# Kernel optimization log

Measured on AMD Instinct MI355X. Metric: run time of the kernel, lower is better.

Reference implementation:

```python
import jax, jax.numpy as jnp
import numpy as np

N_NODES = 100000
N_EDGES = 1000000
D_FEAT = 64


def setup_inputs() -> dict:
    key = jax.random.key(0)
    k1, k2 = jax.random.split(key)
    x = jax.random.normal(k1, (N_NODES, D_FEAT), dtype=jnp.float32)
    es = jax.random.randint(k2, (2, N_EDGES), 0, N_NODES, dtype=jnp.int32)
    return {"x": x, "es": es}


def reference(x, es):
    # message (option='o2i'): col, row = es ; x_i = x[row], x_o = x[col]
    col, row = es[0], es[1]
    x_i = x[row]                              # [E, D]
    x_o = x[col]                              # [E, D]
    msg = jnp.concatenate([x_i, x_o], axis=-1)  # [E, 2D]
    n = x.shape[0]
    # aggregate: scatter-mean over idx=col
    summed = jax.ops.segment_sum(msg, col, num_segments=n)          # [N, 2D]
    ones = jnp.ones((es.shape[1],), dtype=x.dtype)
    count = jax.ops.segment_sum(ones, col, num_segments=n)          # [N]
    count = jnp.maximum(count, 1.0)[:, None]  # clamp(min=1), broadcast
    return summed / count
```

## Files before the change

### kernel.cpp

```cpp
#include <hip/hip_runtime.h>

#define D 64
#define SH 8
#define CPB 256
#define CH 4096
#define MAXNB 512

__global__ __launch_bounds__(256) void count_scan(
    const int* __restrict__ es, int* __restrict__ btot,
    int* __restrict__ done, int* __restrict__ bbase,
    int* __restrict__ cursor, int* __restrict__ offsets,
    int NB, int E, int N) {
  __shared__ int hist[MAXNB];
  __shared__ int sctmp[256];
  __shared__ int lastflag;
  int t = threadIdx.x;
  hist[t] = 0;
  hist[t + 256] = 0;
  __syncthreads();
  int base_e = blockIdx.x * CH;
#pragma unroll
  for (int j = 0; j < 16; j++) {
    int e = base_e + t + j * 256;
    if (e < E) atomicAdd(&hist[es[e] >> SH], 1);
  }
  __syncthreads();
  for (int b = t; b < NB; b += 256) {
    int h = hist[b];
    if (h) atomicAdd(&btot[b], h);
  }
  __syncthreads();
  if (t == 0) {
    __threadfence();
    int d = atomicAdd(done, 1);
    lastflag = (d == (int)gridDim.x - 1);
  }
  __syncthreads();
  if (!lastflag) return;
  __threadfence();
  int i0 = 2 * t, i1 = 2 * t + 1;
  int h0 = (i0 < NB) ? __hip_atomic_load(&btot[i0], __ATOMIC_RELAXED,
                                         __HIP_MEMORY_SCOPE_AGENT) : 0;
  int h1 = (i1 < NB) ? __hip_atomic_load(&btot[i1], __ATOMIC_RELAXED,
                                         __HIP_MEMORY_SCOPE_AGENT) : 0;
  int pair = h0 + h1;
  sctmp[t] = pair;
  __syncthreads();
  for (int off = 1; off < 256; off <<= 1) {
    int v = (t >= off) ? sctmp[t - off] : 0;
    __syncthreads();
    sctmp[t] += v;
    __syncthreads();
  }
  int excl = sctmp[t] - pair;
  if (i0 < NB) { bbase[i0] = excl; cursor[i0] = excl; }
  if (i1 < NB) { bbase[i1] = excl + h0; cursor[i1] = excl + h0; }
  if (t == 0) { bbase[NB] = E; offsets[N] = E; }
}

__global__ __launch_bounds__(256) void scatter_res(
    const int* __restrict__ es, int* __restrict__ cursor,
    int* __restrict__ packed, int NB, int E) {
  __shared__ int hist[MAXNB];
  __shared__ int lstart[MAXNB];
  __shared__ int gbase[MAXNB];
  __shared__ int lcur[MAXNB];
  __shared__ int sctmp[256];
  __shared__ int staged[CH];
  __shared__ unsigned short bidl[CH];
  int t = threadIdx.x;
  hist[t] = 0;
  hist[t + 256] = 0;
  __syncthreads();
  int base_e = blockIdx.x * CH;
  int c[16], r[16];
#pragma unroll
  for (int j = 0; j < 16; j++) {
    int e = base_e + t + j * 256;
    if (e < E) {
      c[j] = es[e];
      r[j] = es[E + e];
      atomicAdd(&hist[c[j] >> SH], 1);
    } else {
      c[j] = -1;
    }
  }
  __syncthreads();
  int h0 = hist[2 * t], h1 = hist[2 * t + 1];
  int pair = h0 + h1;
  sctmp[t] = pair;
  __syncthreads();
  for (int off = 1; off < 256; off <<= 1) {
    int v = (t >= off) ? sctmp[t - off] : 0;
    __syncthreads();
    sctmp[t] += v;
    __syncthreads();
  }
  int excl = sctmp[t] - pair;
  lstart[2 * t] = excl;
  lstart[2 * t + 1] = excl + h0;
  lcur[2 * t] = excl;
  lcur[2 * t + 1] = excl + h0;
  for (int b = t; b < NB; b += 256) {
    int h = hist[b];
    gbase[b] = h ? atomicAdd(&cursor[b], h) : 0;
  }
  __syncthreads();
#pragma unroll
  for (int j = 0; j < 16; j++) {
    if (c[j] >= 0) {
      int b = c[j] >> SH;
      int rank = atomicAdd(&lcur[b], 1);
      staged[rank] = (r[j] << SH) | (c[j] & (CPB - 1));
      bidl[rank] = (unsigned short)b;
    }
  }
  __syncthreads();
  int nloc = min(CH, E - base_e);
  for (int i = t; i < nloc; i += 256) {
    int b = bidl[i];
    packed[gbase[b] + (i - lstart[b])] = staged[i];
  }
}

__global__ __launch_bounds__(256) void sort_cols(
    const int* __restrict__ packed, const int* __restrict__ bbase,
    int* __restrict__ offsets, int* __restrict__ sorted_rows, int N) {
  __shared__ int cnt[CPB];
  __shared__ int sctmp[256];
  __shared__ int cur[CPB];
  int b = blockIdx.x;
  int t = threadIdx.x;
  int s = bbase[b], e = bbase[b + 1];
  cnt[t] = 0;
  __syncthreads();
  for (int i = s + t; i < e; i += 256) atomicAdd(&cnt[packed[i] & (CPB - 1)], 1);
  __syncthreads();
  int v = cnt[t];
  sctmp[t] = v;
  __syncthreads();
  for (int off = 1; off < 256; off <<= 1) {
    int u = (t >= off) ? sctmp[t - off] : 0;
    __syncthreads();
    sctmp[t] += u;
    __syncthreads();
  }
  int excl = sctmp[t] - v;
  cur[t] = excl;
  int gc = (b << SH) + t;
  if (gc < N) offsets[gc] = s + excl;
  __syncthreads();
  for (int i = s + t; i < e; i += 256) {
    int p = packed[i];
    int rank = atomicAdd(&cur[p & (CPB - 1)], 1);
    sorted_rows[s + rank] = p >> SH;
  }
}

__global__ __launch_bounds__(256) void node_reduce(
    const float4* __restrict__ x4, const int* __restrict__ sorted_rows,
    const int* __restrict__ offsets, float* __restrict__ out, int N) {
  int gid = blockIdx.x * 256 + threadIdx.x;
  int node = gid >> 6;
  if (node >= N) return;
  int lane = threadIdx.x & 63;
  int eg = lane >> 4;
  int d16 = lane & 15;
  int start = offsets[node];
  int cnt = offsets[node + 1] - start;
  float4 a0 = make_float4(0.f, 0.f, 0.f, 0.f);
  float4 a1 = make_float4(0.f, 0.f, 0.f, 0.f);
  float4 a2 = make_float4(0.f, 0.f, 0.f, 0.f);
  float4 a3 = make_float4(0.f, 0.f, 0.f, 0.f);
  for (int base = 0; base < cnt; base += 16) {
    int k0 = base + eg;
    int k1 = base + 4 + eg;
    int k2 = base + 8 + eg;
    int k3 = base + 12 + eg;
    int r0 = (k0 < cnt) ? sorted_rows[start + k0] : -1;
    int r1 = (k1 < cnt) ? sorted_rows[start + k1] : -1;
    int r2 = (k2 < cnt) ? sorted_rows[start + k2] : -1;
    int r3 = (k3 < cnt) ? sorted_rows[start + k3] : -1;
    if (r0 >= 0) { float4 v = x4[(size_t)r0 * 16 + d16];
      a0.x += v.x; a0.y += v.y; a0.z += v.z; a0.w += v.w; }
    if (r1 >= 0) { float4 v = x4[(size_t)r1 * 16 + d16];
      a1.x += v.x; a1.y += v.y; a1.z += v.z; a1.w += v.w; }
    if (r2 >= 0) { float4 v = x4[(size_t)r2 * 16 + d16];
      a2.x += v.x; a2.y += v.y; a2.z += v.z; a2.w += v.w; }
    if (r3 >= 0) { float4 v = x4[(size_t)r3 * 16 + d16];
      a3.x += v.x; a3.y += v.y; a3.z += v.z; a3.w += v.w; }
  }
  a0.x += a1.x + a2.x + a3.x;
  a0.y += a1.y + a2.y + a3.y;
  a0.z += a1.z + a2.z + a3.z;
  a0.w += a1.w + a2.w + a3.w;
  a0.x += __shfl_xor(a0.x, 16); a0.y += __shfl_xor(a0.y, 16);
  a0.z += __shfl_xor(a0.z, 16); a0.w += __shfl_xor(a0.w, 16);
  a0.x += __shfl_xor(a0.x, 32); a0.y += __shfl_xor(a0.y, 32);
  a0.z += __shfl_xor(a0.z, 32); a0.w += __shfl_xor(a0.w, 32);
  float4* o4 = (float4*)(out + (size_t)node * 2 * D);
  if (eg == 0) {
    float inv = 1.0f / (float)(cnt > 0 ? cnt : 1);
    a0.x *= inv; a0.y *= inv; a0.z *= inv; a0.w *= inv;
    o4[d16] = a0;
  } else if (eg == 1) {
    float4 v = (cnt > 0) ? x4[(size_t)node * 16 + d16]
                         : make_float4(0.f, 0.f, 0.f, 0.f);
    o4[16 + d16] = v;
  }
}


__global__ __launch_bounds__(256) void edge_scatter_atomic(
    const int* __restrict__ es, const float* __restrict__ x,
    float* __restrict__ out, int* __restrict__ count, int E) {
  int gid = blockIdx.x * blockDim.x + threadIdx.x;
  int e = gid >> 6;
  int lane = gid & 63;
  if (e >= E) return;
  int c = es[e];
  int r = es[E + e];
  if (lane == 0) atomicAdd(&count[c], 1);
  float v = x[(size_t)r * D + lane];
  unsafeAtomicAdd(&out[(size_t)c * 2 * D + lane], v);
}

__global__ __launch_bounds__(256) void finalize_atomic(
    const float* __restrict__ x, float* __restrict__ out,
    const int* __restrict__ count, int N) {
  int gid = blockIdx.x * blockDim.x + threadIdx.x;
  int node = gid >> 5;
  int j4 = gid & 31;
  if (node >= N) return;
  int cnt = count[node];
  float4* out4 = (float4*)(out + (size_t)node * 2 * D);
  if (j4 < 16) {
    float4 s = out4[j4];
    float inv = 1.0f / (float)(cnt > 0 ? cnt : 1);
    s.x *= inv; s.y *= inv; s.z *= inv; s.w *= inv;
    out4[j4] = s;
  } else {
    float4 v;
    if (cnt > 0) {
      const float4* x4 = (const float4*)(x + (size_t)node * D);
      v = x4[j4 - 16];
    } else {
      v = make_float4(0.f, 0.f, 0.f, 0.f);
    }
    out4[j4] = v;
  }
}

extern "C" void kernel_launch(void* const* d_in, const int* in_sizes, int n_in,
                              void* d_out, int out_size, void* d_ws, size_t ws_size,
                              hipStream_t stream) {
  const float* x = (const float*)d_in[0];
  const int* es = (const int*)d_in[1];
  int N = in_sizes[0] / D;
  int E = in_sizes[1] / 2;
  float* out = (float*)d_out;

  int NB = (N + CPB - 1) >> SH;
  int NBLK = (E + CH - 1) / CH;
  size_t need = ((size_t)NB + 1 + (NB + 1) + NB + ((size_t)N + 1) +
                 2 * (size_t)E) * sizeof(int);
  if (NB > MAXNB || ws_size < need) {
    int* count = (int*)d_ws;
    hipMemsetAsync(count, 0, (size_t)N * sizeof(int), stream);
    hipMemsetAsync(out, 0, (size_t)N * 2 * D * sizeof(float), stream);
    long long t1 = (long long)E * 64;
    edge_scatter_atomic<<<(int)((t1 + 255) / 256), 256, 0, stream>>>(es, x, out, count, E);
    long long t2 = (long long)N * 32;
    finalize_atomic<<<(int)((t2 + 255) / 256), 256, 0, stream>>>(x, out, count, N);
    return;
  }

  int* ws = (int*)d_ws;
  int* btot = ws;
  int* done = btot + NB;
  int* bbase = done + 1;
  int* cursor = bbase + NB + 1;
  int* offsets = cursor + NB;
  int* packed = offsets + N + 1;
  int* sorted_rows = packed + E;

  hipMemsetAsync(btot, 0, ((size_t)NB + 1) * sizeof(int), stream);

  count_scan<<<NBLK, 256, 0, stream>>>(es, btot, done, bbase, cursor, offsets,
                                       NB, E, N);
  scatter_res<<<NBLK, 256, 0, stream>>>(es, cursor, packed, NB, E);
  sort_cols<<<NB, 256, 0, stream>>>(packed, bbase, offsets, sorted_rows, N);

  long long rt = (long long)N * 64;
  node_reduce<<<(int)((rt + 255) / 256), 256, 0, stream>>>(
      (const float4*)x, sorted_rows, offsets, out, N);
}
```

Baseline: 163.4 us.

## Sort edges into 16-node groups by source-row key and reduce with LDS atomics

Replaces the per-column counting sort and per-node gather reduction with a sort into 16-node groups. Inside each group, edges are ordered by the high bits of the source row so gathers of x rows are more local. A wavefront then processes each group and accumulates into padded shared-memory rows with LDS float atomics, which gives better load balance across nodes and more cache locality for gathers. The cost is many shared-memory atomics per element and a lower-parallelism write-out loop.

```diff
diff --git a/kernel.cpp b/kernel.cpp
--- a/kernel.cpp
+++ b/kernel.cpp
@@ -9,8 +9,7 @@
 __global__ __launch_bounds__(256) void count_scan(
     const int* __restrict__ es, int* __restrict__ btot,
     int* __restrict__ done, int* __restrict__ bbase,
-    int* __restrict__ cursor, int* __restrict__ offsets,
-    int NB, int E, int N) {
+    int* __restrict__ cursor, int NB, int E) {
   __shared__ int hist[MAXNB];
   __shared__ int sctmp[256];
   __shared__ int lastflag;
@@ -55,7 +54,7 @@
   int excl = sctmp[t] - pair;
   if (i0 < NB) { bbase[i0] = excl; cursor[i0] = excl; }
   if (i1 < NB) { bbase[i1] = excl + h0; cursor[i1] = excl + h0; }
-  if (t == 0) { bbase[NB] = E; offsets[N] = E; }
+  if (t == 0) bbase[NB] = E;
 }
 
 __global__ __launch_bounds__(256) void scatter_res(
@@ -123,90 +122,114 @@
   }
 }
 
-__global__ __launch_bounds__(256) void sort_cols(
+__global__ __launch_bounds__(256) void sort_grp(
     const int* __restrict__ packed, const int* __restrict__ bbase,
-    int* __restrict__ offsets, int* __restrict__ sorted_rows, int N) {
-  __shared__ int cnt[CPB];
+    int* __restrict__ goff, int* __restrict__ cnts,
+    int* __restrict__ spk, int N, int E, int NB) {
+  __shared__ int kh[1024];
+  __shared__ int kcur[1024];
+  __shared__ int ncnt[256];
   __shared__ int sctmp[256];
-  __shared__ int cur[CPB];
   int b = blockIdx.x;
   int t = threadIdx.x;
   int s = bbase[b], e = bbase[b + 1];
-  cnt[t] = 0;
-  __syncthreads();
-  for (int i = s + t; i < e; i += 256) atomicAdd(&cnt[packed[i] & (CPB - 1)], 1);
-  __syncthreads();
-  int v = cnt[t];
-  sctmp[t] = v;
-  __syncthreads();
-  for (int off = 1; off < 256; off <<= 1) {
-    int u = (t >= off) ? sctmp[t - off] : 0;
-    __syncthreads();
-    sctmp[t] += u;
-    __syncthreads();
-  }
-  int excl = sctmp[t] - v;
-  cur[t] = excl;
-  int gc = (b << SH) + t;
-  if (gc < N) offsets[gc] = s + excl;
+  kh[t] = 0; kh[t + 256] = 0; kh[t + 512] = 0; kh[t + 768] = 0;
+  ncnt[t] = 0;
   __syncthreads();
   for (int i = s + t; i < e; i += 256) {
     int p = packed[i];
-    int rank = atomicAdd(&cur[p & (CPB - 1)], 1);
-    sorted_rows[s + rank] = p >> SH;
-  }
-}
-
-__global__ __launch_bounds__(256) void node_reduce(
-    const float4* __restrict__ x4, const int* __restrict__ sorted_rows,
-    const int* __restrict__ offsets, float* __restrict__ out, int N) {
-  int gid = blockIdx.x * 256 + threadIdx.x;
-  int node = gid >> 6;
-  if (node >= N) return;
-  int lane = threadIdx.x & 63;
-  int eg = lane >> 4;
-  int d16 = lane & 15;
-  int start = offsets[node];
-  int cnt = offsets[node + 1] - start;
-  float4 a0 = make_float4(0.f, 0.f, 0.f, 0.f);
-  float4 a1 = make_float4(0.f, 0.f, 0.f, 0.f);
-  float4 a2 = make_float4(0.f, 0.f, 0.f, 0.f);
-  float4 a3 = make_float4(0.f, 0.f, 0.f, 0.f);
-  for (int base = 0; base < cnt; base += 16) {
-    int k0 = base + eg;
-    int k1 = base + 4 + eg;
-    int k2 = base + 8 + eg;
-    int k3 = base + 12 + eg;
-    int r0 = (k0 < cnt) ? sorted_rows[start + k0] : -1;
-    int r1 = (k1 < cnt) ? sorted_rows[start + k1] : -1;
-    int r2 = (k2 < cnt) ? sorted_rows[start + k2] : -1;
-    int r3 = (k3 < cnt) ? sorted_rows[start + k3] : -1;
-    if (r0 >= 0) { float4 v = x4[(size_t)r0 * 16 + d16];
-      a0.x += v.x; a0.y += v.y; a0.z += v.z; a0.w += v.w; }
-    if (r1 >= 0) { float4 v = x4[(size_t)r1 * 16 + d16];
-      a1.x += v.x; a1.y += v.y; a1.z += v.z; a1.w += v.w; }
-    if (r2 >= 0) { float4 v = x4[(size_t)r2 * 16 + d16];
-      a2.x += v.x; a2.y += v.y; a2.z += v.z; a2.w += v.w; }
-    if (r3 >= 0) { float4 v = x4[(size_t)r3 * 16 + d16];
-      a3.x += v.x; a3.y += v.y; a3.z += v.z; a3.w += v.w; }
-  }
-  a0.x += a1.x + a2.x + a3.x;
-  a0.y += a1.y + a2.y + a3.y;
-  a0.z += a1.z + a2.z + a3.z;
-  a0.w += a1.w + a2.w + a3.w;
-  a0.x += __shfl_xor(a0.x, 16); a0.y += __shfl_xor(a0.y, 16);
-  a0.z += __shfl_xor(a0.z, 16); a0.w += __shfl_xor(a0.w, 16);
-  a0.x += __shfl_xor(a0.x, 32); a0.y += __shfl_xor(a0.y, 32);
-  a0.z += __shfl_xor(a0.z, 32); a0.w += __shfl_xor(a0.w, 32);
-  float4* o4 = (float4*)(out + (size_t)node * 2 * D);
-  if (eg == 0) {
-    float inv = 1.0f / (float)(cnt > 0 ? cnt : 1);
-    a0.x *= inv; a0.y *= inv; a0.z *= inv; a0.w *= inv;
-    o4[d16] = a0;
-  } else if (eg == 1) {
-    float4 v = (cnt > 0) ? x4[(size_t)node * 16 + d16]
-                         : make_float4(0.f, 0.f, 0.f, 0.f);
-    o4[16 + d16] = v;
+    int d8 = p & 255;
+    int key = ((d8 >> 4) << 6) | ((p >> 8) >> 11);
+    atomicAdd(&kh[key], 1);
+    atomicAdd(&ncnt[d8], 1);
+  }
+  __syncthreads();
+  int k0 = kh[4 * t], k1 = kh[4 * t + 1], k2 = kh[4 * t + 2], k3 = kh[4 * t + 3];
+  int sum = k0 + k1 + k2 + k3;
+  sctmp[t] = sum;
+  __syncthreads();
+  for (int off = 1; off < 256; off <<= 1) {
+    int v = (t >= off) ? sctmp[t - off] : 0;
+    __syncthreads();
+    sctmp[t] += v;
+    __syncthreads();
+  }
+  int excl = sctmp[t] - sum;
+  kcur[4 * t] = excl;
+  kcur[4 * t + 1] = excl + k0;
+  kcur[4 * t + 2] = excl + k0 + k1;
+  kcur[4 * t + 3] = excl + k0 + k1 + k2;
+  int node = (b << 8) + t;
+  if (node < N) cnts[node] = ncnt[t];
+  __syncthreads();
+  if (t < 16) goff[b * 16 + t] = s + kcur[t * 64];
+  if (b == NB - 1 && t == 0) goff[NB * 16] = E;
+  __syncthreads();
+  for (int i = s + t; i < e; i += 256) {
+    int p = packed[i];
+    int key = (((p & 255) >> 4) << 6) | ((p >> 8) >> 11);
+    int rank = atomicAdd(&kcur[key], 1);
+    spk[s + rank] = p;
+  }
+}
+
+#define ASTR 65
+__global__ __launch_bounds__(256) void node_reduce_grp(
+    const float4* __restrict__ x4, const int* __restrict__ spk,
+    const int* __restrict__ goff, const int* __restrict__ cnts,
+    float* __restrict__ out, int N, int NG) {
+  __shared__ float acc[4][16 * ASTR];
+  int t = threadIdx.x;
+  int w = t >> 6;
+  int lane = t & 63;
+  int g = blockIdx.x * 4 + w;
+  if (g >= NG) return;
+  float* aw = acc[w];
+  for (int i = lane; i < 16 * ASTR; i += 64) aw[i] = 0.f;
+  int s = goff[g], e = goff[g + 1];
+  int eg = lane >> 4, d16 = lane & 15;
+  for (int base = s; base < e; base += 16) {
+    int i0 = base + eg, i1 = base + 4 + eg;
+    int i2 = base + 8 + eg, i3 = base + 12 + eg;
+    int p0 = (i0 < e) ? spk[i0] : -1;
+    int p1 = (i1 < e) ? spk[i1] : -1;
+    int p2 = (i2 < e) ? spk[i2] : -1;
+    int p3 = (i3 < e) ? spk[i3] : -1;
+    if (p0 >= 0) { float4 v = x4[(size_t)(p0 >> 8) * 16 + d16];
+      float* a = &aw[(p0 & 15) * ASTR + d16 * 4];
+      atomicAdd(a + 0, v.x); atomicAdd(a + 1, v.y);
+      atomicAdd(a + 2, v.z); atomicAdd(a + 3, v.w); }
+    if (p1 >= 0) { float4 v = x4[(size_t)(p1 >> 8) * 16 + d16];
+      float* a = &aw[(p1 & 15) * ASTR + d16 * 4];
+      atomicAdd(a + 0, v.x); atomicAdd(a + 1, v.y);
+      atomicAdd(a + 2, v.z); atomicAdd(a + 3, v.w); }
+    if (p2 >= 0) { float4 v = x4[(size_t)(p2 >> 8) * 16 + d16];
+      float* a = &aw[(p2 & 15) * ASTR + d16 * 4];
+      atomicAdd(a + 0, v.x); atomicAdd(a + 1, v.y);
+      atomicAdd(a + 2, v.z); atomicAdd(a + 3, v.w); }
+    if (p3 >= 0) { float4 v = x4[(size_t)(p3 >> 8) * 16 + d16];
+      float* a = &aw[(p3 & 15) * ASTR + d16 * 4];
+      atomicAdd(a + 0, v.x); atomicAdd(a + 1, v.y);
+      atomicAdd(a + 2, v.z); atomicAdd(a + 3, v.w); }
+  }
+  int sub = lane >> 5;
+  int l5 = lane & 31;
+  int h = l5 >> 4;
+  int dd = l5 & 15;
+  for (int n = 0; n < 16; n += 2) {
+    int node = g * 16 + n + sub;
+    if (node >= N) continue;
+    int cn = cnts[node];
+    float4* o4 = (float4*)(out + (size_t)node * 2 * D);
+    if (h == 0) {
+      float inv = 1.0f / (float)(cn > 0 ? cn : 1);
+      float* a = &aw[(n + sub) * ASTR + dd * 4];
+      o4[dd] = make_float4(a[0] * inv, a[1] * inv, a[2] * inv, a[3] * inv);
+    } else {
+      float4 v = (cn > 0) ? x4[(size_t)node * 16 + dd]
+                          : make_float4(0.f, 0.f, 0.f, 0.f);
+      o4[16 + dd] = v;
+    }
   }
 }
 
@@ -262,8 +285,9 @@
 
   int NB = (N + CPB - 1) >> SH;
   int NBLK = (E + CH - 1) / CH;
-  size_t need = ((size_t)NB + 1 + (NB + 1) + NB + ((size_t)N + 1) +
-                 2 * (size_t)E) * sizeof(int);
+  int NG = (N + 15) / 16;
+  size_t need = ((size_t)NB + 1 + (NB + 1) + NB + (size_t)N +
+                 ((size_t)NB * 16 + 1) + 2 * (size_t)E) * sizeof(int);
   if (NB > MAXNB || ws_size < need) {
     int* count = (int*)d_ws;
     hipMemsetAsync(count, 0, (size_t)N * sizeof(int), stream);
@@ -280,18 +304,16 @@
   int* done = btot + NB;
   int* bbase = done + 1;
   int* cursor = bbase + NB + 1;
-  int* offsets = cursor + NB;
-  int* packed = offsets + N + 1;
-  int* sorted_rows = packed + E;
+  int* cnts = cursor + NB;
+  int* goff = cnts + N;
+  int* packed = goff + NB * 16 + 1;
+  int* spk = packed + E;
 
   hipMemsetAsync(btot, 0, ((size_t)NB + 1) * sizeof(int), stream);
 
-  count_scan<<<NBLK, 256, 0, stream>>>(es, btot, done, bbase, cursor, offsets,
-                                       NB, E, N);
+  count_scan<<<NBLK, 256, 0, stream>>>(es, btot, done, bbase, cursor, NB, E);
   scatter_res<<<NBLK, 256, 0, stream>>>(es, cursor, packed, NB, E);
-  sort_cols<<<NB, 256, 0, stream>>>(packed, bbase, offsets, sorted_rows, N);
-
-  long long rt = (long long)N * 64;
-  node_reduce<<<(int)((rt + 255) / 256), 256, 0, stream>>>(
-      (const float4*)x, sorted_rows, offsets, out, N);
-}
+  sort_grp<<<NB, 256, 0, stream>>>(packed, bbase, goff, cnts, spk, N, E, NB);
+  node_reduce_grp<<<(NG + 3) / 4, 256, 0, stream>>>(
+      (const float4*)x, spk, goff, cnts, out, N, NG);
+}
```

Result: slower. 494.1 us (+202.4%).

## Process four nodes per wave with prefetched row indices in node_reduce

Applied to the files above, without the earlier changes.

The node reduction kernel now has each 64-lane wave handle four consecutive nodes instead of one. The offsets for all four nodes are loaded once and broadcast with shuffles. The first 16 sorted row indices of the next node are prefetched while the current node is being accumulated, so index-load latency overlaps with the gathers. This gives fewer waves and more per-wave memory-level parallelism, at the cost of fewer resident waves overall and some serialisation across the four nodes.

```diff
diff --git a/kernel.cpp b/kernel.cpp
--- a/kernel.cpp
+++ b/kernel.cpp
@@ -157,56 +157,88 @@
   }
 }
 
-__global__ __launch_bounds__(256) void node_reduce(
+__global__ __launch_bounds__(256) void node_reduce4(
     const float4* __restrict__ x4, const int* __restrict__ sorted_rows,
     const int* __restrict__ offsets, float* __restrict__ out, int N) {
-  int gid = blockIdx.x * 256 + threadIdx.x;
-  int node = gid >> 6;
-  if (node >= N) return;
+  int wid = (blockIdx.x * 256 + threadIdx.x) >> 6;
+  int nb = wid * 4;
+  if (nb >= N) return;
   int lane = threadIdx.x & 63;
   int eg = lane >> 4;
   int d16 = lane & 15;
-  int start = offsets[node];
-  int cnt = offsets[node + 1] - start;
-  float4 a0 = make_float4(0.f, 0.f, 0.f, 0.f);
-  float4 a1 = make_float4(0.f, 0.f, 0.f, 0.f);
-  float4 a2 = make_float4(0.f, 0.f, 0.f, 0.f);
-  float4 a3 = make_float4(0.f, 0.f, 0.f, 0.f);
-  for (int base = 0; base < cnt; base += 16) {
-    int k0 = base + eg;
-    int k1 = base + 4 + eg;
-    int k2 = base + 8 + eg;
-    int k3 = base + 12 + eg;
-    int r0 = (k0 < cnt) ? sorted_rows[start + k0] : -1;
-    int r1 = (k1 < cnt) ? sorted_rows[start + k1] : -1;
-    int r2 = (k2 < cnt) ? sorted_rows[start + k2] : -1;
-    int r3 = (k3 < cnt) ? sorted_rows[start + k3] : -1;
-    if (r0 >= 0) { float4 v = x4[(size_t)r0 * 16 + d16];
+  int l3 = lane & 3;
+  int ia = nb + l3;       if (ia > N) ia = N;
+  int ib = nb + l3 + 1;   if (ib > N) ib = N;
+  int oa = offsets[ia];
+  int ob = offsets[ib];
+  int s = __shfl(oa, 0), e = __shfl(ob, 0);
+  int p0 = (s + eg < e)      ? sorted_rows[s + eg]      : -1;
+  int p1 = (s + 4 + eg < e)  ? sorted_rows[s + 4 + eg]  : -1;
+  int p2 = (s + 8 + eg < e)  ? sorted_rows[s + 8 + eg]  : -1;
+  int p3 = (s + 12 + eg < e) ? sorted_rows[s + 12 + eg] : -1;
+#pragma unroll
+  for (int n = 0; n < 4; n++) {
+    int node = nb + n;
+    int cnt = e - s;
+    int c0 = p0, c1 = p1, c2 = p2, c3 = p3;
+    int sc = s;
+    if (n < 3) {
+      s = __shfl(oa, n + 1); e = __shfl(ob, n + 1);
+      p0 = (s + eg < e)      ? sorted_rows[s + eg]      : -1;
+      p1 = (s + 4 + eg < e)  ? sorted_rows[s + 4 + eg]  : -1;
+      p2 = (s + 8 + eg < e)  ? sorted_rows[s + 8 + eg]  : -1;
+      p3 = (s + 12 + eg < e) ? sorted_rows[s + 12 + eg] : -1;
+    }
+    if (node >= N) continue;
+    float4 cpv = make_float4(0.f, 0.f, 0.f, 0.f);
+    if (eg == 1) cpv = x4[(size_t)node * 16 + d16];
+    float4 a0 = make_float4(0.f, 0.f, 0.f, 0.f);
+    float4 a1 = make_float4(0.f, 0.f, 0.f, 0.f);
+    float4 a2 = make_float4(0.f, 0.f, 0.f, 0.f);
+    float4 a3 = make_float4(0.f, 0.f, 0.f, 0.f);
+    if (c0 >= 0) { float4 v = x4[(size_t)c0 * 16 + d16];
       a0.x += v.x; a0.y += v.y; a0.z += v.z; a0.w += v.w; }
-    if (r1 >= 0) { float4 v = x4[(size_t)r1 * 16 + d16];
+    if (c1 >= 0) { float4 v = x4[(size_t)c1 * 16 + d16];
       a1.x += v.x; a1.y += v.y; a1.z += v.z; a1.w += v.w; }
-    if (r2 >= 0) { float4 v = x4[(size_t)r2 * 16 + d16];
+    if (c2 >= 0) { float4 v = x4[(size_t)c2 * 16 + d16];
       a2.x += v.x; a2.y += v.y; a2.z += v.z; a2.w += v.w; }
-    if (r3 >= 0) { float4 v = x4[(size_t)r3 * 16 + d16];
+    if (c3 >= 0) { float4 v = x4[(size_t)c3 * 16 + d16];
       a3.x += v.x; a3.y += v.y; a3.z += v.z; a3.w += v.w; }
-  }
-  a0.x += a1.x + a2.x + a3.x;
-  a0.y += a1.y + a2.y + a3.y;
-  a0.z += a1.z + a2.z + a3.z;
-  a0.w += a1.w + a2.w + a3.w;
-  a0.x += __shfl_xor(a0.x, 16); a0.y += __shfl_xor(a0.y, 16);
-  a0.z += __shfl_xor(a0.z, 16); a0.w += __shfl_xor(a0.w, 16);
-  a0.x += __shfl_xor(a0.x, 32); a0.y += __shfl_xor(a0.y, 32);
-  a0.z += __shfl_xor(a0.z, 32); a0.w += __shfl_xor(a0.w, 32);
-  float4* o4 = (float4*)(out + (size_t)node * 2 * D);
-  if (eg == 0) {
-    float inv = 1.0f / (float)(cnt > 0 ? cnt : 1);
-    a0.x *= inv; a0.y *= inv; a0.z *= inv; a0.w *= inv;
-    o4[d16] = a0;
-  } else if (eg == 1) {
-    float4 v = (cnt > 0) ? x4[(size_t)node * 16 + d16]
-                         : make_float4(0.f, 0.f, 0.f, 0.f);
-    o4[16 + d16] = v;
+    for (int base = 16; base < cnt; base += 16) {
+      int k0 = sc + base + eg;
+      int k1 = sc + base + 4 + eg;
+      int k2 = sc + base + 8 + eg;
+      int k3 = sc + base + 12 + eg;
+      int r0 = (k0 - sc < cnt) ? sorted_rows[k0] : -1;
+      int r1 = (k1 - sc < cnt) ? sorted_rows[k1] : -1;
+      int r2 = (k2 - sc < cnt) ? sorted_rows[k2] : -1;
+      int r3 = (k3 - sc < cnt) ? sorted_rows[k3] : -1;
+      if (r0 >= 0) { float4 v = x4[(size_t)r0 * 16 + d16];
+        a0.x += v.x; a0.y += v.y; a0.z += v.z; a0.w += v.w; }
+      if (r1 >= 0) { float4 v = x4[(size_t)r1 * 16 + d16];
+        a1.x += v.x; a1.y += v.y; a1.z += v.z; a1.w += v.w; }
+      if (r2 >= 0) { float4 v = x4[(size_t)r2 * 16 + d16];
+        a2.x += v.x; a2.y += v.y; a2.z += v.z; a2.w += v.w; }
+      if (r3 >= 0) { float4 v = x4[(size_t)r3 * 16 + d16];
+        a3.x += v.x; a3.y += v.y; a3.z += v.z; a3.w += v.w; }
+    }
+    a0.x += a1.x + a2.x + a3.x;
+    a0.y += a1.y + a2.y + a3.y;
+    a0.z += a1.z + a2.z + a3.z;
+    a0.w += a1.w + a2.w + a3.w;
+    a0.x += __shfl_xor(a0.x, 16); a0.y += __shfl_xor(a0.y, 16);
+    a0.z += __shfl_xor(a0.z, 16); a0.w += __shfl_xor(a0.w, 16);
+    a0.x += __shfl_xor(a0.x, 32); a0.y += __shfl_xor(a0.y, 32);
+    a0.z += __shfl_xor(a0.z, 32); a0.w += __shfl_xor(a0.w, 32);
+    float4* o4 = (float4*)(out + (size_t)node * 2 * D);
+    if (eg == 0) {
+      float inv = 1.0f / (float)(cnt > 0 ? cnt : 1);
+      a0.x *= inv; a0.y *= inv; a0.z *= inv; a0.w *= inv;
+      o4[d16] = a0;
+    } else if (eg == 1) {
+      if (cnt <= 0) cpv = make_float4(0.f, 0.f, 0.f, 0.f);
+      o4[16 + d16] = cpv;
+    }
   }
 }
 
@@ -291,7 +323,8 @@
   scatter_res<<<NBLK, 256, 0, stream>>>(es, cursor, packed, NB, E);
   sort_cols<<<NB, 256, 0, stream>>>(packed, bbase, offsets, sorted_rows, N);
 
-  long long rt = (long long)N * 64;
-  node_reduce<<<(int)((rt + 255) / 256), 256, 0, stream>>>(
+  int waves = (N + 3) / 4;
+  int blocks = (waves + 3) / 4;
+  node_reduce4<<<blocks, 256, 0, stream>>>(
       (const float4*)x, sorted_rows, offsets, out, N);
 }
```

Result: no change. 161.0 us (-1.5%).
